# Optimization experiments

Hardware: AMD Instinct MI355X
Metric: run time of the kernel (lower is better)

The kernel has to match this reference:

```python
import jax, jax.numpy as jnp
import numpy as np

T, B, I, H = 256, 32, 128, 256
CLIP = 2.0

def setup_inputs() -> dict:
    key = jax.random.key(0)
    ks = jax.random.split(key, 10)
    si, sh = 1.0 / np.sqrt(I), 1.0 / np.sqrt(H)
    return {
        "x":     jax.random.normal(ks[0], (T, B, I), jnp.float32),
        "Wx":    jax.random.normal(ks[1], (4 * H, I), jnp.float32) * si,
        "bx":    jax.random.normal(ks[2], (4 * H,), jnp.float32) * si,
        "Wh":    jax.random.normal(ks[3], (4 * H, H), jnp.float32) * sh,
        "bh":    jax.random.normal(ks[4], (4 * H,), jnp.float32) * sh,
        "w_mod": jax.random.normal(ks[5], (1, H), jnp.float32) * sh,
        "b_mod": jax.random.normal(ks[6], (1,), jnp.float32) * sh,
        "w_fan": jax.random.normal(ks[7], (H, 1), jnp.float32),
        "b_fan": jax.random.normal(ks[8], (H,), jnp.float32),
        "alpha": 1e-4 * jax.random.uniform(ks[9], (H, H), jnp.float32),
    }

def reference(x, Wx, bx, Wh, bh, w_mod, b_mod, w_fan, b_fan, alpha):
    Bn = x.shape[1]
    # precompute input projection for all timesteps: [T, B, 4H]
    xf = jnp.einsum('tbi,gi->tbg', x, Wx) + bx

    def step(state, xf_t):
        h, c, hebb = state  # h,c: [B,H]; hebb: [B,H,H]
        fioj = xf_t + h @ Wh.T + bh                     # [B,4H]
        f = jax.nn.sigmoid(fioj[:, :H])
        i = jax.nn.sigmoid(fioj[:, H:2 * H])
        o = jax.nn.sigmoid(fioj[:, 2 * H:3 * H])
        # h_pred @ (alpha * hebb) : batched vec-mat product
        plast = jnp.einsum('bh,hk,bhk->bk', h, alpha, hebb)
        j = jnp.tanh(fioj[:, 3 * H:] + plast)
        c_new = f * c + i * j
        h_new = o * jnp.tanh(c_new)
        eta = jnp.tanh(c_new @ w_mod.T + b_mod)          # [B,1]
        myeta = eta * w_fan[:, 0] + b_fan                # [B,H] (Linear(1,H) fanout)
        # delta_hebb = outer(h_pred, j); eta modulates along the j axis
        hebb_new = jnp.clip(hebb + myeta[:, None, :] * (h[:, :, None] * j[:, None, :]),
                            -CLIP, CLIP)
        return (h_new, c_new, hebb_new), h_new

    init = (jnp.zeros((Bn, H), jnp.float32),
            jnp.zeros((Bn, H), jnp.float32),
            jnp.zeros((Bn, H, H), jnp.float32))
    (h, c, hebb), hs = jax.lax.scan(step, init, xf)
    return hs, h, c, hebb
```

## Files before the change

### kernel.cpp

```cpp
#include <hip/hip_runtime.h>


#define TT 256
#define BB 32
#define II 128
#define HH 256
#define G4 1024

typedef _Float16 h2_t __attribute__((ext_vector_type(2)));
typedef unsigned long long u64;

__device__ __forceinline__ float sigm(float x) {
    return 1.0f / (1.0f + __expf(-x));
}
__device__ __forceinline__ float tanhfast(float x) {
    return 1.0f - 2.0f / (__expf(2.0f * x) + 1.0f);
}
__device__ __forceinline__ unsigned pkh(float lo, float hi) {
    h2_t v;
    v.x = (_Float16)lo;
    v.y = (_Float16)hi;
    return __builtin_bit_cast(unsigned, v);
}

#if __has_builtin(__builtin_amdgcn_fdot2)
__device__ __forceinline__ float dot2(unsigned a, unsigned b, float c) {
    return __builtin_amdgcn_fdot2(__builtin_bit_cast(h2_t, a),
                                  __builtin_bit_cast(h2_t, b), c, false);
}
#else
__device__ __forceinline__ float dot2(unsigned a, unsigned b, float c) {
    h2_t av = __builtin_bit_cast(h2_t, a), bv = __builtin_bit_cast(h2_t, b);
    return c + (float)av.x * (float)bv.x + (float)av.y * (float)bv.y;
}
#endif

__device__ __forceinline__ h2_t pkfma(h2_t a, h2_t b, h2_t c) {
#if __has_builtin(__builtin_elementwise_fma)
    return __builtin_elementwise_fma(a, b, c);
#else
    return a * b + c;
#endif
}
__device__ __forceinline__ h2_t clip2h(h2_t x) {
    const h2_t lo = {(_Float16)-2.0f, (_Float16)-2.0f};
    const h2_t hi = {(_Float16)2.0f, (_Float16)2.0f};
#if __has_builtin(__builtin_elementwise_max) && __has_builtin(__builtin_elementwise_min)
    return __builtin_elementwise_min(__builtin_elementwise_max(x, lo), hi);
#else
    h2_t r = x;
    r.x = r.x < lo.x ? lo.x : (r.x > hi.x ? hi.x : r.x);
    r.y = r.y < lo.y ? lo.y : (r.y > hi.y ? hi.y : r.y);
    return r;
#endif
}

__global__ __launch_bounds__(256) void prep_wd3(const float* __restrict__ Wh,
                                                uint4* __restrict__ Wd3) {
    int idx = blockIdx.x * 256 + threadIdx.x;
    int ro = idx >> 12, rem = idx & 4095;
    int g = rem >> 2, ri = rem & 3;
    int r8 = 4 * ro + ri;
    const float4* s = (const float4*)(Wh + (size_t)g * HH + (r8 << 3));
    float4 a = s[0], b2 = s[1];
    uint4 o;
    o.x = pkh(a.x, a.y);
    o.y = pkh(a.z, a.w);
    o.z = pkh(b2.x, b2.y);
    o.w = pkh(b2.z, b2.w);
    Wd3[idx] = o;
}

__global__ __launch_bounds__(256) void prep_alq(const float* __restrict__ alpha,
                                                uint4* __restrict__ alQ) {
    int idx = blockIdx.x * 256 + threadIdx.x;
    int p4 = idx >> 8, k = idx & 255;
    unsigned r[4];
#pragma unroll
    for (int j = 0; j < 4; ++j) {
        int p = 4 * p4 + j;
        float a0 = alpha[(size_t)(2 * p) * HH + k];
        float a1 = alpha[(size_t)(2 * p + 1) * HH + k];
        r[j] = pkh(a0, a1);
    }
    uint4 o; o.x = r[0]; o.y = r[1]; o.z = r[2]; o.w = r[3];
    alQ[idx] = o;
}

__global__ __launch_bounds__(256) void xf_gemm(const float* __restrict__ x,
                                               const float* __restrict__ Wx,
                                               const float* __restrict__ bx,
                                               const float* __restrict__ bh,
                                               float* __restrict__ xf) {
    __shared__ float As[64][37];
    __shared__ float Bs[64][37];
    const int tid = threadIdx.x;
    const int tx = tid & 15, ty = tid >> 4;
    const int m0 = blockIdx.y << 6;
    const int n0 = blockIdx.x << 6;
    float c[4][4] = {};

    for (int k0 = 0; k0 < II; k0 += 32) {
#pragma unroll
        for (int hh = 0; hh < 2; ++hh) {
            int row = (tid >> 3) + (hh << 5);
            int col = (tid & 7) << 2;
            float4 va = *(const float4*)(x + (size_t)(m0 + row) * II + k0 + col);
            As[row][col] = va.x; As[row][col + 1] = va.y;
            As[row][col + 2] = va.z; As[row][col + 3] = va.w;
            float4 vb = *(const float4*)(Wx + (size_t)(n0 + row) * II + k0 + col);
            Bs[row][col] = vb.x; Bs[row][col + 1] = vb.y;
            Bs[row][col + 2] = vb.z; Bs[row][col + 3] = vb.w;
        }
        __syncthreads();
#pragma unroll
        for (int kk = 0; kk < 32; ++kk) {
            float a[4], bb[4];
#pragma unroll
            for (int u = 0; u < 4; ++u) a[u] = As[(ty << 2) + u][kk];
#pragma unroll
            for (int v = 0; v < 4; ++v) bb[v] = Bs[(tx << 2) + v][kk];
#pragma unroll
            for (int u = 0; u < 4; ++u)
#pragma unroll
                for (int v = 0; v < 4; ++v)
                    c[u][v] = fmaf(a[u], bb[v], c[u][v]);
        }
        __syncthreads();
    }
    const int n = n0 + (tx << 2);
    float4 bxv = *(const float4*)(bx + n);
    float4 bhv = *(const float4*)(bh + n);
    float4 badd = {bxv.x + bhv.x, bxv.y + bhv.y, bxv.z + bhv.z, bxv.w + bhv.w};
#pragma unroll
    for (int u = 0; u < 4; ++u) {
        int m = m0 + (ty << 2) + u;
        float4 o = {c[u][0] + badd.x, c[u][1] + badd.y,
                    c[u][2] + badd.z, c[u][3] + badd.w};
        *(float4*)(xf + (size_t)m * G4 + n) = o;
    }
}

#define HBQ_FOREACH(X) X(0) X(1) X(2) X(3) X(4) X(5) X(6) X(7)

#define HBQ_DECL(i) h2_t hp##i = {(_Float16)0.0f, (_Float16)0.0f};
#define HBQ_OUT(i) \
    hbout[(size_t)(r0g + 2 * i) * HH + k]     = (float)hp##i.x; \
    hbout[(size_t)(r0g + 2 * i + 1) * HH + k] = (float)hp##i.y;

#define HBQ_STEP(i, au, hou, hnu) { \
    h2_t al2 = __builtin_bit_cast(h2_t, au); \
    h2_t ho2 = __builtin_bit_cast(h2_t, hou); \
    h2_t hn2 = __builtin_bit_cast(h2_t, hnu); \
    hp##i = clip2h(pkfma(mj2, ho2, hp##i)); \
    h2_t hna = hn2 * al2; \
    pp = dot2(__builtin_bit_cast(unsigned, hna), \
              __builtin_bit_cast(unsigned, hp##i), pp); }

#define HBQ_CHUNK(q, AV, i0, i1, i2, i3) { \
    uint4 ho = hfO4[hb4 + (q)]; \
    uint4 hn = hfN4[hb4 + (q)]; \
    HBQ_STEP(i0, AV.x, ho.x, hn.x) \
    HBQ_STEP(i1, AV.y, ho.y, hn.y) \
    HBQ_STEP(i2, AV.z, ho.z, hn.z) \
    HBQ_STEP(i3, AV.w, ho.w, hn.w) }

#define HBV_STEP(i, hou) { \
    h2_t ho2 = __builtin_bit_cast(h2_t, hou); \
    hp##i = clip2h(pkfma(mj2, ho2, hp##i)); }
#define HBV_CHUNK(q, i0, i1, i2, i3) { \
    uint4 ho = hfO4[hb4 + (q)]; \
    HBV_STEP(i0, ho.x) HBV_STEP(i1, ho.y) \
    HBV_STEP(i2, ho.z) HBV_STEP(i3, ho.w) }

#define DOTW(W, HV) { \
    ac0 = dot2(W.x, HV.x, ac0); ac1 = dot2(W.y, HV.y, ac1); \
    ac2 = dot2(W.z, HV.z, ac2); ac3 = dot2(W.w, HV.w, ac3); }

__global__ __launch_bounds__(1024, 1) void scan_kernel(
    const float* __restrict__ xf,
    const uint4* __restrict__ Wd3,
    const uint4* __restrict__ alQ,
    const float* __restrict__ w_mod,
    const float* __restrict__ b_mod,
    const float* __restrict__ w_fan,
    const float* __restrict__ b_fan,
    u64* __restrict__ exData,
    float* __restrict__ out) {
    const int bid = blockIdx.x;
    const int r   = bid >> 5;
    const int b   = bid & 31;
    const int tid = threadIdx.x;
    const int k   = tid & (HH - 1);
    const int rg  = tid >> 8;
    const int r0g = r * 64 + rg * 16;
    const int hb4 = r0g >> 3;

    __shared__ alignas(16) unsigned short hf_s[2][HH];
    __shared__ float fioj_s[G4];
    __shared__ float pp_s[4][HH];
    __shared__ float red_s[4];

    HBQ_FOREACH(HBQ_DECL)

    if (tid < HH) {
        hf_s[0][tid] = 0;
        hf_s[1][tid] = 0;
    }
    if (tid < 4) red_s[tid] = 0.0f;
    __syncthreads();

    const float bmod = b_mod[0];
    const float wf = w_fan[k], bf = b_fan[k], wm = w_mod[k];
    float creg = 0.0f, jreg = 0.0f, hnreg = 0.0f;

    const uint4* wb = Wd3 + ((size_t)(2 * r) << 12) + (tid << 2);
    uint4 w0 = wb[0], w1 = wb[1], w2 = wb[2], w3 = wb[3];
    uint4 w4 = wb[4096], w5 = wb[4097], w6 = wb[4098], w7 = wb[4099];
    uint4 aqA = alQ[(size_t)(8 * r + 2 * rg) * 256 + k];
    uint4 aqB = alQ[(size_t)(8 * r + 2 * rg + 1) * 256 + k];

    const float* xfp = xf + (size_t)b * G4 + tid;

    u64* myEx = exData + (size_t)((b * 4 + r) * 2) * 1024;
    const u64* pEx1 = exData + (size_t)((b * 4 + ((r + 1) & 3)) * 2) * 1024;
    const u64* pEx2 = exData + (size_t)((b * 4 + ((r + 2) & 3)) * 2) * 1024;
    const u64* pEx3 = exData + (size_t)((b * 4 + ((r + 3) & 3)) * 2) * 1024;

    for (int t = 0; t < TT; ++t) {
        float xfv = 0.0f;
        if (rg == r) xfv = xfp[(size_t)t * BB * G4];

        float eta = tanhfast(((red_s[0] + red_s[1]) + (red_s[2] + red_s[3])) + bmod);
        float mj = fmaf(eta, wf, bf) * jreg;
        h2_t mj2;
        mj2.x = (_Float16)mj;
        mj2.y = mj2.x;
        const uint4* hfO4 = (const uint4*)hf_s[t & 1];
        const uint4* hfN4 = (const uint4*)hf_s[(t & 1) ^ 1];
        float pp = 0.0f;
        HBQ_CHUNK(0, aqA, 0, 1, 2, 3)
        HBQ_CHUNK(1, aqB, 4, 5, 6, 7)
        pp_s[rg][k] = pp;

        float ac0 = 0.f, ac1 = 0.f, ac2 = 0.f, ac3 = 0.f;
        {
            const int hx = r << 3;
            uint4 h0 = hfN4[hx], h1 = hfN4[hx + 1];
            uint4 h2 = hfN4[hx + 2], h3 = hfN4[hx + 3];
            DOTW(w0, h0) DOTW(w1, h1) DOTW(w2, h2) DOTW(w3, h3)
            uint4 h4 = hfN4[hx + 4], h5 = hfN4[hx + 5];
            uint4 h6 = hfN4[hx + 6], h7 = hfN4[hx + 7];
            DOTW(w4, h4) DOTW(w5, h5) DOTW(w6, h6) DOTW(w7, h7)
        }
        float part = ((ac0 + ac1) + (ac2 + ac3)) + xfv;
        __syncthreads();

        if (tid >= 768) {
            int k2 = tid - 768;
            part += (pp_s[0][k2] + pp_s[1][k2]) + (pp_s[2][k2] + pp_s[3][k2]);
        }

        const unsigned tag = (unsigned)(t + 1);
        const int off = (t & 1) * 1024 + tid;
        {
            u64 pkv = ((u64)tag << 32) |
                      (u64)__builtin_bit_cast(unsigned, part);
            __hip_atomic_store(&myEx[off], pkv, __ATOMIC_RELAXED,
                               __HIP_MEMORY_SCOPE_AGENT);
        }

        {
            float s1 = 0.f, s2 = 0.f, s3 = 0.f;
            bool d1 = false, d2 = false, d3 = false;
            do {
                if (!d1) {
                    u64 v = __hip_atomic_load(&pEx1[off], __ATOMIC_RELAXED,
                                              __HIP_MEMORY_SCOPE_AGENT);
                    if ((unsigned)(v >> 32) == tag) {
                        s1 = __builtin_bit_cast(float, (unsigned)v);
                        d1 = true;
                    }
                }
                if (!d2) {
                    u64 v = __hip_atomic_load(&pEx2[off], __ATOMIC_RELAXED,
                                              __HIP_MEMORY_SCOPE_AGENT);
                    if ((unsigned)(v >> 32) == tag) {
                        s2 = __builtin_bit_cast(float, (unsigned)v);
                        d2 = true;
                    }
                }
                if (!d3) {
                    u64 v = __hip_atomic_load(&pEx3[off], __ATOMIC_RELAXED,
                                              __HIP_MEMORY_SCOPE_AGENT);
                    if ((unsigned)(v >> 32) == tag) {
                        s3 = __builtin_bit_cast(float, (unsigned)v);
                        d3 = true;
                    }
                }
            } while (!(d1 && d2 && d3));
            fioj_s[tid] = part + ((s1 + s2) + s3);
        }
        __syncthreads();

        float fg = sigm(fioj_s[k]);
        float ig = sigm(fioj_s[HH + k]);
        float og = sigm(fioj_s[2 * HH + k]);
        float jp = fioj_s[3 * HH + k];
        jreg = tanhfast(jp);
        creg = fmaf(fg, creg, ig * jreg);
        hnreg = og * tanhfast(creg);
        if (rg == 0) {
            _Float16 hh = (_Float16)hnreg;
            hf_s[t & 1][k] = __builtin_bit_cast(unsigned short, hh);
            if (r == 0) out[((size_t)t * BB + b) * HH + k] = hnreg;
            float e = creg * wm;
#pragma unroll
            for (int m = 32; m >= 1; m >>= 1) e += __shfl_xor(e, m, 64);
            if ((k & 63) == 0) red_s[k >> 6] = e;
        }
        __syncthreads();
    }

    {
        float eta = tanhfast(((red_s[0] + red_s[1]) + (red_s[2] + red_s[3])) + bmod);
        float mj = fmaf(eta, wf, bf) * jreg;
        h2_t mj2;
        mj2.x = (_Float16)mj;
        mj2.y = mj2.x;
        const uint4* hfO4 = (const uint4*)hf_s[0];
        HBV_CHUNK(0, 0, 1, 2, 3)
        HBV_CHUNK(1, 4, 5, 6, 7)
    }

    const size_t HS = (size_t)TT * BB * HH;
    if (r == 0 && rg == 0) {
        out[HS + (size_t)b * HH + k]           = hnreg;
        out[HS + BB * HH + (size_t)b * HH + k] = creg;
    }
    float* hbout = out + HS + 2 * BB * HH + (size_t)b * HH * HH;
    HBQ_FOREACH(HBQ_OUT)
}

extern "C" void kernel_launch(void* const* d_in, const int* in_sizes, int n_in,
                              void* d_out, int out_size, void* d_ws,
                              size_t ws_size, hipStream_t stream) {
    const float* x     = (const float*)d_in[0];
    const float* Wx    = (const float*)d_in[1];
    const float* bx    = (const float*)d_in[2];
    const float* Wh    = (const float*)d_in[3];
    const float* bh    = (const float*)d_in[4];
    const float* w_mod = (const float*)d_in[5];
    const float* b_mod = (const float*)d_in[6];
    const float* w_fan = (const float*)d_in[7];
    const float* b_fan = (const float*)d_in[8];
    const float* alpha = (const float*)d_in[9];
    float* out = (float*)d_out;

    float* xf  = (float*)d_ws;
    uint4* Wd3 = (uint4*)((char*)d_ws + 33554432);
    uint4* alQ = (uint4*)((char*)d_ws + 34078720);
    u64*   exD = (u64*)((char*)d_ws + 34209792);

    hipLaunchKernelGGL(prep_wd3, dim3(128), dim3(256), 0, stream, Wh, Wd3);
    hipLaunchKernelGGL(prep_alq, dim3(32), dim3(256), 0, stream, alpha, alQ);
    hipLaunchKernelGGL(xf_gemm, dim3(16, 128), dim3(256), 0, stream,
                       x, Wx, bx, bh, xf);
    hipLaunchKernelGGL(scan_kernel, dim3(128), dim3(1024), 0, stream,
                       xf, Wd3, alQ, w_mod, b_mod, w_fan, b_fan,
                       exD, out);
}
```

Before: 838.5 us.

## Split each batch's recurrence across two blocks instead of four

Each batch element's scan now runs on 2 workgroups (64 total) instead of 4. Each block keeps a 128-column slice of Wh in registers (16 uint4 per thread) and stages its alpha slice in LDS. The cross-block exchange now talks to one partner, with pp partials published separately so they can be summed remotely. The next step's xf value is prefetched one step ahead. This cuts inter-block synchronisation and the number of polled locations per step, at the cost of doubled per-block dot-product and hebbian work, higher register and LDS pressure, and fewer CUs in use.

```diff
diff --git a/kernel.cpp b/kernel.cpp
--- a/kernel.cpp
+++ b/kernel.cpp
@@ -55,36 +55,29 @@
 #endif
 }
 
-__global__ __launch_bounds__(256) void prep_wd3(const float* __restrict__ Wh,
-                                                uint4* __restrict__ Wd3) {
+__global__ __launch_bounds__(256) void prep_wd2(const float* __restrict__ Wh,
+                                                uint4* __restrict__ Wd2) {
     int idx = blockIdx.x * 256 + threadIdx.x;
-    int ro = idx >> 12, rem = idx & 4095;
-    int g = rem >> 2, ri = rem & 3;
-    int r8 = 4 * ro + ri;
-    const float4* s = (const float4*)(Wh + (size_t)g * HH + (r8 << 3));
+    int Q = idx >> 10, g = idx & 1023;
+    const float4* s = (const float4*)(Wh + (size_t)g * HH + (Q << 3));
     float4 a = s[0], b2 = s[1];
     uint4 o;
     o.x = pkh(a.x, a.y);
     o.y = pkh(a.z, a.w);
     o.z = pkh(b2.x, b2.y);
     o.w = pkh(b2.z, b2.w);
-    Wd3[idx] = o;
-}
-
-__global__ __launch_bounds__(256) void prep_alq(const float* __restrict__ alpha,
-                                                uint4* __restrict__ alQ) {
+    Wd2[idx] = o;
+}
+
+__global__ __launch_bounds__(256) void prep_alp(const float* __restrict__ alpha,
+                                                unsigned* __restrict__ alP) {
     int idx = blockIdx.x * 256 + threadIdx.x;
-    int p4 = idx >> 8, k = idx & 255;
-    unsigned r[4];
-#pragma unroll
-    for (int j = 0; j < 4; ++j) {
-        int p = 4 * p4 + j;
-        float a0 = alpha[(size_t)(2 * p) * HH + k];
-        float a1 = alpha[(size_t)(2 * p + 1) * HH + k];
-        r[j] = pkh(a0, a1);
-    }
-    uint4 o; o.x = r[0]; o.y = r[1]; o.z = r[2]; o.w = r[3];
-    alQ[idx] = o;
+    int r = idx >> 14, rem = idx & 16383;
+    int j = rem & 1, kk = (rem >> 1) & 255, pg = rem >> 9;
+    int row0 = r * 128 + 4 * pg + 2 * j;
+    float a0 = alpha[(size_t)row0 * HH + kk];
+    float a1 = alpha[(size_t)(row0 + 1) * HH + kk];
+    alP[idx] = pkh(a0, a1);
 }
 
 __global__ __launch_bounds__(256) void xf_gemm(const float* __restrict__ x,
@@ -141,7 +134,8 @@
     }
 }
 
-#define HBQ_FOREACH(X) X(0) X(1) X(2) X(3) X(4) X(5) X(6) X(7)
+#define HBQ_FOREACH(X) X(0) X(1) X(2) X(3) X(4) X(5) X(6) X(7) \
+                       X(8) X(9) X(10) X(11) X(12) X(13) X(14) X(15)
 
 #define HBQ_DECL(i) h2_t hp##i = {(_Float16)0.0f, (_Float16)0.0f};
 #define HBQ_OUT(i) \
@@ -157,13 +151,15 @@
     pp = dot2(__builtin_bit_cast(unsigned, hna), \
               __builtin_bit_cast(unsigned, hp##i), pp); }
 
-#define HBQ_CHUNK(q, AV, i0, i1, i2, i3) { \
+#define HBQ_CHUNK(q, i0, i1, i2, i3) { \
     uint4 ho = hfO4[hb4 + (q)]; \
     uint4 hn = hfN4[hb4 + (q)]; \
-    HBQ_STEP(i0, AV.x, ho.x, hn.x) \
-    HBQ_STEP(i1, AV.y, ho.y, hn.y) \
-    HBQ_STEP(i2, AV.z, ho.z, hn.z) \
-    HBQ_STEP(i3, AV.w, ho.w, hn.w) }
+    uint2 A0 = *(const uint2*)&als[((((rg << 3) + 2 * (q)) << 8) + k) << 1]; \
+    uint2 A1 = *(const uint2*)&als[((((rg << 3) + 2 * (q) + 1) << 8) + k) << 1]; \
+    HBQ_STEP(i0, A0.x, ho.x, hn.x) \
+    HBQ_STEP(i1, A0.y, ho.y, hn.y) \
+    HBQ_STEP(i2, A1.x, ho.z, hn.z) \
+    HBQ_STEP(i3, A1.y, ho.w, hn.w) }
 
 #define HBV_STEP(i, hou) { \
     h2_t ho2 = __builtin_bit_cast(h2_t, hou); \
@@ -179,8 +175,8 @@
 
 __global__ __launch_bounds__(1024, 1) void scan_kernel(
     const float* __restrict__ xf,
-    const uint4* __restrict__ Wd3,
-    const uint4* __restrict__ alQ,
+    const uint4* __restrict__ Wd2,
+    const unsigned* __restrict__ alP,
     const float* __restrict__ w_mod,
     const float* __restrict__ b_mod,
     const float* __restrict__ w_fan,
@@ -193,16 +189,25 @@
     const int tid = threadIdx.x;
     const int k   = tid & (HH - 1);
     const int rg  = tid >> 8;
-    const int r0g = r * 64 + rg * 16;
-    const int hb4 = r0g >> 3;
+    const int r0g = (r << 7) + (rg << 5);
+    const int hb4 = (r << 4) + (rg << 2);
 
     __shared__ alignas(16) unsigned short hf_s[2][HH];
-    __shared__ float fioj_s[G4];
+    __shared__ alignas(16) float fioj_s[G4];
     __shared__ float pp_s[4][HH];
     __shared__ float red_s[4];
+    __shared__ alignas(16) unsigned als[16384];
 
     HBQ_FOREACH(HBQ_DECL)
 
+    {
+        const uint4* s4 = (const uint4*)(alP + ((size_t)r << 14));
+        uint4* d4 = (uint4*)als;
+        d4[tid]        = s4[tid];
+        d4[tid + 1024] = s4[tid + 1024];
+        d4[tid + 2048] = s4[tid + 2048];
+        d4[tid + 3072] = s4[tid + 3072];
+    }
     if (tid < HH) {
         hf_s[0][tid] = 0;
         hf_s[1][tid] = 0;
@@ -214,22 +219,25 @@
     const float wf = w_fan[k], bf = b_fan[k], wm = w_mod[k];
     float creg = 0.0f, jreg = 0.0f, hnreg = 0.0f;
 
-    const uint4* wb = Wd3 + ((size_t)(2 * r) << 12) + (tid << 2);
-    uint4 w0 = wb[0], w1 = wb[1], w2 = wb[2], w3 = wb[3];
-    uint4 w4 = wb[4096], w5 = wb[4097], w6 = wb[4098], w7 = wb[4099];
-    uint4 aqA = alQ[(size_t)(8 * r + 2 * rg) * 256 + k];
-    uint4 aqB = alQ[(size_t)(8 * r + 2 * rg + 1) * 256 + k];
-
+    const uint4* wb = Wd2 + ((size_t)r << 14) + tid;
+    uint4 w0 = wb[0],      w1 = wb[1024],  w2 = wb[2048],  w3 = wb[3072];
+    uint4 w4 = wb[4096],   w5 = wb[5120],  w6 = wb[6144],  w7 = wb[7168];
+    uint4 w8 = wb[8192],   w9 = wb[9216],  w10 = wb[10240], w11 = wb[11264];
+    uint4 w12 = wb[12288], w13 = wb[13312], w14 = wb[14336], w15 = wb[15360];
+
+    const bool hasxf = ((tid >> 9) == r);
     const float* xfp = xf + (size_t)b * G4 + tid;
-
-    u64* myEx = exData + (size_t)((b * 4 + r) * 2) * 1024;
-    const u64* pEx1 = exData + (size_t)((b * 4 + ((r + 1) & 3)) * 2) * 1024;
-    const u64* pEx2 = exData + (size_t)((b * 4 + ((r + 2) & 3)) * 2) * 1024;
-    const u64* pEx3 = exData + (size_t)((b * 4 + ((r + 3) & 3)) * 2) * 1024;
+    float xcur = hasxf ? xfp[0] : 0.0f;
+
+    u64* myEx = exData + ((size_t)(b * 2 + r) << 12);
+    const u64* pEx = exData + ((size_t)(b * 2 + (r ^ 1)) << 12);
 
     for (int t = 0; t < TT; ++t) {
-        float xfv = 0.0f;
-        if (rg == r) xfv = xfp[(size_t)t * BB * G4];
+        float xnext = 0.0f;
+        if (hasxf && t + 1 < TT) xnext = xfp[(size_t)(t + 1) * BB * G4];
+
+        const unsigned tag = (unsigned)(t + 1);
+        const int off = (t & 1) * 2048;
 
         float eta = tanhfast(((red_s[0] + red_s[1]) + (red_s[2] + red_s[3])) + bmod);
         float mj = fmaf(eta, wf, bf) * jreg;
@@ -239,43 +247,70 @@
         const uint4* hfO4 = (const uint4*)hf_s[t & 1];
         const uint4* hfN4 = (const uint4*)hf_s[(t & 1) ^ 1];
         float pp = 0.0f;
-        HBQ_CHUNK(0, aqA, 0, 1, 2, 3)
-        HBQ_CHUNK(1, aqB, 4, 5, 6, 7)
+        HBQ_CHUNK(0, 0, 1, 2, 3)
+        HBQ_CHUNK(1, 4, 5, 6, 7)
+        HBQ_CHUNK(2, 8, 9, 10, 11)
+        HBQ_CHUNK(3, 12, 13, 14, 15)
         pp_s[rg][k] = pp;
+        __hip_atomic_store(&myEx[off + 1024 + tid],
+                           ((u64)tag << 32) |
+                               (u64)__builtin_bit_cast(unsigned, pp),
+                           __ATOMIC_RELAXED, __HIP_MEMORY_SCOPE_AGENT);
 
         float ac0 = 0.f, ac1 = 0.f, ac2 = 0.f, ac3 = 0.f;
         {
-            const int hx = r << 3;
-            uint4 h0 = hfN4[hx], h1 = hfN4[hx + 1];
-            uint4 h2 = hfN4[hx + 2], h3 = hfN4[hx + 3];
-            DOTW(w0, h0) DOTW(w1, h1) DOTW(w2, h2) DOTW(w3, h3)
-            uint4 h4 = hfN4[hx + 4], h5 = hfN4[hx + 5];
-            uint4 h6 = hfN4[hx + 6], h7 = hfN4[hx + 7];
-            DOTW(w4, h4) DOTW(w5, h5) DOTW(w6, h6) DOTW(w7, h7)
+            const uint4* hv = hfN4 + (r << 4);
+            uint4 hA = hv[0], hB = hv[1];
+            DOTW(w0, hA) DOTW(w1, hB)
+            hA = hv[2]; hB = hv[3];
+            DOTW(w2, hA) DOTW(w3, hB)
+            hA = hv[4]; hB = hv[5];
+            DOTW(w4, hA) DOTW(w5, hB)
+            hA = hv[6]; hB = hv[7];
+            DOTW(w6, hA) DOTW(w7, hB)
+            hA = hv[8]; hB = hv[9];
+            DOTW(w8, hA) DOTW(w9, hB)
+            hA = hv[10]; hB = hv[11];
+            DOTW(w10, hA) DOTW(w11, hB)
+            hA = hv[12]; hB = hv[13];
+            DOTW(w12, hA) DOTW(w13, hB)
+            hA = hv[14]; hB = hv[15];
+            DOTW(w14, hA) DOTW(w15, hB)
         }
-        float part = ((ac0 + ac1) + (ac2 + ac3)) + xfv;
+        float part = ((ac0 + ac1) + (ac2 + ac3)) + xcur;
+        xcur = xnext;
+
+        __hip_atomic_store(&myEx[off + tid],
+                           ((u64)tag << 32) |
+                               (u64)__builtin_bit_cast(unsigned, part),
+                           __ATOMIC_RELAXED, __HIP_MEMORY_SCOPE_AGENT);
         __syncthreads();
 
-        if (tid >= 768) {
-            int k2 = tid - 768;
-            part += (pp_s[0][k2] + pp_s[1][k2]) + (pp_s[2][k2] + pp_s[3][k2]);
-        }
-
-        const unsigned tag = (unsigned)(t + 1);
-        const int off = (t & 1) * 1024 + tid;
-        {
-            u64 pkv = ((u64)tag << 32) |
-                      (u64)__builtin_bit_cast(unsigned, part);
-            __hip_atomic_store(&myEx[off], pkv, __ATOMIC_RELAXED,
-                               __HIP_MEMORY_SCOPE_AGENT);
-        }
-
-        {
-            float s1 = 0.f, s2 = 0.f, s3 = 0.f;
-            bool d1 = false, d2 = false, d3 = false;
+        float fv;
+        if (tid < 768) {
+            u64 v;
+            for (;;) {
+                v = __hip_atomic_load(&pEx[off + tid], __ATOMIC_RELAXED,
+                                      __HIP_MEMORY_SCOPE_AGENT);
+                if ((unsigned)(v >> 32) == tag) break;
+            }
+            fv = part + __builtin_bit_cast(float, (unsigned)v);
+        } else {
+            float own = (pp_s[0][k] + pp_s[1][k]) + (pp_s[2][k] + pp_s[3][k]);
+            float s0 = 0.f, s1 = 0.f, s2 = 0.f, s3 = 0.f, s4 = 0.f;
+            bool d0 = false, d1 = false, d2 = false, d3 = false, d4 = false;
             do {
+                if (!d0) {
+                    u64 v = __hip_atomic_load(&pEx[off + tid], __ATOMIC_RELAXED,
+                                              __HIP_MEMORY_SCOPE_AGENT);
+                    if ((unsigned)(v >> 32) == tag) {
+                        s0 = __builtin_bit_cast(float, (unsigned)v);
+                        d0 = true;
+                    }
+                }
                 if (!d1) {
-                    u64 v = __hip_atomic_load(&pEx1[off], __ATOMIC_RELAXED,
+                    u64 v = __hip_atomic_load(&pEx[off + 1024 + k],
+                                              __ATOMIC_RELAXED,
                                               __HIP_MEMORY_SCOPE_AGENT);
                     if ((unsigned)(v >> 32) == tag) {
                         s1 = __builtin_bit_cast(float, (unsigned)v);
@@ -283,7 +318,8 @@
                     }
                 }
                 if (!d2) {
-                    u64 v = __hip_atomic_load(&pEx2[off], __ATOMIC_RELAXED,
+                    u64 v = __hip_atomic_load(&pEx[off + 1280 + k],
+                                              __ATOMIC_RELAXED,
                                               __HIP_MEMORY_SCOPE_AGENT);
                     if ((unsigned)(v >> 32) == tag) {
                         s2 = __builtin_bit_cast(float, (unsigned)v);
@@ -291,16 +327,27 @@
                     }
                 }
                 if (!d3) {
-                    u64 v = __hip_atomic_load(&pEx3[off], __ATOMIC_RELAXED,
+                    u64 v = __hip_atomic_load(&pEx[off + 1536 + k],
+                                              __ATOMIC_RELAXED,
                                               __HIP_MEMORY_SCOPE_AGENT);
                     if ((unsigned)(v >> 32) == tag) {
                         s3 = __builtin_bit_cast(float, (unsigned)v);
                         d3 = true;
                     }
                 }
-            } while (!(d1 && d2 && d3));
-            fioj_s[tid] = part + ((s1 + s2) + s3);
+                if (!d4) {
+                    u64 v = __hip_atomic_load(&pEx[off + 1792 + k],
+                                              __ATOMIC_RELAXED,
+                                              __HIP_MEMORY_SCOPE_AGENT);
+                    if ((unsigned)(v >> 32) == tag) {
+                        s4 = __builtin_bit_cast(float, (unsigned)v);
+                        d4 = true;
+                    }
+                }
+            } while (!(d0 && d1 && d2 && d3 && d4));
+            fv = (part + own) + (((s0 + s1) + (s2 + s3)) + s4);
         }
+        fioj_s[tid] = fv;
         __syncthreads();
 
         float fg = sigm(fioj_s[k]);
@@ -331,6 +378,8 @@
         const uint4* hfO4 = (const uint4*)hf_s[0];
         HBV_CHUNK(0, 0, 1, 2, 3)
         HBV_CHUNK(1, 4, 5, 6, 7)
+        HBV_CHUNK(2, 8, 9, 10, 11)
+        HBV_CHUNK(3, 12, 13, 14, 15)
     }
 
     const size_t HS = (size_t)TT * BB * HH;
@@ -357,16 +406,16 @@
     const float* alpha = (const float*)d_in[9];
     float* out = (float*)d_out;
 
-    float* xf  = (float*)d_ws;
-    uint4* Wd3 = (uint4*)((char*)d_ws + 33554432);
-    uint4* alQ = (uint4*)((char*)d_ws + 34078720);
-    u64*   exD = (u64*)((char*)d_ws + 34209792);
-
-    hipLaunchKernelGGL(prep_wd3, dim3(128), dim3(256), 0, stream, Wh, Wd3);
-    hipLaunchKernelGGL(prep_alq, dim3(32), dim3(256), 0, stream, alpha, alQ);
+    float*    xf  = (float*)d_ws;
+    uint4*    Wd2 = (uint4*)((char*)d_ws + 33554432);
+    unsigned* alP = (unsigned*)((char*)d_ws + 34078720);
+    u64*      exD = (u64*)((char*)d_ws + 34209792);
+
+    hipLaunchKernelGGL(prep_wd2, dim3(128), dim3(256), 0, stream, Wh, Wd2);
+    hipLaunchKernelGGL(prep_alp, dim3(128), dim3(256), 0, stream, alpha, alP);
     hipLaunchKernelGGL(xf_gemm, dim3(16, 128), dim3(256), 0, stream,
                        x, Wx, bx, bh, xf);
-    hipLaunchKernelGGL(scan_kernel, dim3(128), dim3(1024), 0, stream,
-                       xf, Wd3, alQ, w_mod, b_mod, w_fan, b_fan,
+    hipLaunchKernelGGL(scan_kernel, dim3(64), dim3(1024), 0, stream,
+                       xf, Wd2, alP, w_mod, b_mod, w_fan, b_fan,
                        exD, out);
 }
```

Result: slower. 1.088 ms (+29.7%).

## Speed up cross-block exchange with dual-buffer publish and sc0 polling loads

Applied to the files above, without the earlier changes.

Each partial sum is now written twice, once with workgroup scope to a second buffer and once with agent scope to the original buffer. Peers poll the fast buffer with inline-asm sc0 global loads and fall back to agent-scope atomic loads every fourth iteration. The non-plastic partials are published before the block barrier, the next timestep's xf value is prefetched, and gate math is limited to the threads that use it. The goal is lower inter-block handshake latency per step, but it relies on cache-coherence behaviour that is not formally guaranteed and adds extra stores and workspace.

```diff
diff --git a/kernel.cpp b/kernel.cpp
--- a/kernel.cpp
+++ b/kernel.cpp
@@ -53,6 +53,18 @@
     r.y = r.y < lo.y ? lo.y : (r.y > hi.y ? hi.y : r.y);
     return r;
 #endif
+}
+
+__device__ __forceinline__ void ld3_fast(const u64* p1, const u64* p2,
+                                         const u64* p3,
+                                         u64& v1, u64& v2, u64& v3) {
+    asm volatile(
+        "global_load_dwordx2 %0, %3, off sc0\n\t"
+        "global_load_dwordx2 %1, %4, off sc0\n\t"
+        "global_load_dwordx2 %2, %5, off sc0\n\t"
+        "s_waitcnt vmcnt(0)"
+        : "=&v"(v1), "=&v"(v2), "=&v"(v3)
+        : "v"(p1), "v"(p2), "v"(p3));
 }
 
 __global__ __launch_bounds__(256) void prep_wd3(const float* __restrict__ Wh,
@@ -177,6 +189,13 @@
     ac0 = dot2(W.x, HV.x, ac0); ac1 = dot2(W.y, HV.y, ac1); \
     ac2 = dot2(W.z, HV.z, ac2); ac3 = dot2(W.w, HV.w, ac3); }
 
+#define PUBLISH(val) { \
+    u64 pkv = ((u64)tag << 32) | (u64)__builtin_bit_cast(unsigned, val); \
+    __hip_atomic_store(&myF[off], pkv, __ATOMIC_RELAXED, \
+                       __HIP_MEMORY_SCOPE_WORKGROUP); \
+    __hip_atomic_store(&myEx[off], pkv, __ATOMIC_RELAXED, \
+                       __HIP_MEMORY_SCOPE_AGENT); }
+
 __global__ __launch_bounds__(1024, 1) void scan_kernel(
     const float* __restrict__ xf,
     const uint4* __restrict__ Wd3,
@@ -186,6 +205,7 @@
     const float* __restrict__ w_fan,
     const float* __restrict__ b_fan,
     u64* __restrict__ exData,
+    u64* __restrict__ exFast,
     float* __restrict__ out) {
     const int bid = blockIdx.x;
     const int r   = bid >> 5;
@@ -221,15 +241,23 @@
     uint4 aqB = alQ[(size_t)(8 * r + 2 * rg + 1) * 256 + k];
 
     const float* xfp = xf + (size_t)b * G4 + tid;
+    float xcur = (rg == r) ? xfp[0] : 0.0f;
 
     u64* myEx = exData + (size_t)((b * 4 + r) * 2) * 1024;
     const u64* pEx1 = exData + (size_t)((b * 4 + ((r + 1) & 3)) * 2) * 1024;
     const u64* pEx2 = exData + (size_t)((b * 4 + ((r + 2) & 3)) * 2) * 1024;
     const u64* pEx3 = exData + (size_t)((b * 4 + ((r + 3) & 3)) * 2) * 1024;
+    u64* myF = exFast + (size_t)((b * 4 + r) * 2) * 1024;
+    const u64* pF1 = exFast + (size_t)((b * 4 + ((r + 1) & 3)) * 2) * 1024;
+    const u64* pF2 = exFast + (size_t)((b * 4 + ((r + 2) & 3)) * 2) * 1024;
+    const u64* pF3 = exFast + (size_t)((b * 4 + ((r + 3) & 3)) * 2) * 1024;
 
     for (int t = 0; t < TT; ++t) {
-        float xfv = 0.0f;
-        if (rg == r) xfv = xfp[(size_t)t * BB * G4];
+        float xnext = 0.0f;
+        if (rg == r && t + 1 < TT) xnext = xfp[(size_t)(t + 1) * BB * G4];
+
+        const unsigned tag = (unsigned)(t + 1);
+        const int off = (t & 1) * 1024 + tid;
 
         float eta = tanhfast(((red_s[0] + red_s[1]) + (red_s[2] + red_s[3])) + bmod);
         float mj = fmaf(eta, wf, bf) * jreg;
@@ -253,64 +281,62 @@
             uint4 h6 = hfN4[hx + 6], h7 = hfN4[hx + 7];
             DOTW(w4, h4) DOTW(w5, h5) DOTW(w6, h6) DOTW(w7, h7)
         }
-        float part = ((ac0 + ac1) + (ac2 + ac3)) + xfv;
+        float part = ((ac0 + ac1) + (ac2 + ac3)) + xcur;
+        xcur = xnext;
+
+        if (tid < 768) PUBLISH(part)
         __syncthreads();
 
         if (tid >= 768) {
             int k2 = tid - 768;
             part += (pp_s[0][k2] + pp_s[1][k2]) + (pp_s[2][k2] + pp_s[3][k2]);
-        }
-
-        const unsigned tag = (unsigned)(t + 1);
-        const int off = (t & 1) * 1024 + tid;
-        {
-            u64 pkv = ((u64)tag << 32) |
-                      (u64)__builtin_bit_cast(unsigned, part);
-            __hip_atomic_store(&myEx[off], pkv, __ATOMIC_RELAXED,
-                               __HIP_MEMORY_SCOPE_AGENT);
+            PUBLISH(part)
         }
 
         {
             float s1 = 0.f, s2 = 0.f, s3 = 0.f;
             bool d1 = false, d2 = false, d3 = false;
+            const u64* f1 = pF1 + off;
+            const u64* f2 = pF2 + off;
+            const u64* f3 = pF3 + off;
+            int it = 0;
             do {
-                if (!d1) {
-                    u64 v = __hip_atomic_load(&pEx1[off], __ATOMIC_RELAXED,
-                                              __HIP_MEMORY_SCOPE_AGENT);
-                    if ((unsigned)(v >> 32) == tag) {
-                        s1 = __builtin_bit_cast(float, (unsigned)v);
-                        d1 = true;
-                    }
+                u64 v1, v2, v3;
+                if ((it & 3) != 3) {
+                    ld3_fast(f1, f2, f3, v1, v2, v3);
+                } else {
+                    v1 = __hip_atomic_load(pEx1 + off, __ATOMIC_RELAXED,
+                                           __HIP_MEMORY_SCOPE_AGENT);
+                    v2 = __hip_atomic_load(pEx2 + off, __ATOMIC_RELAXED,
+                                           __HIP_MEMORY_SCOPE_AGENT);
+                    v3 = __hip_atomic_load(pEx3 + off, __ATOMIC_RELAXED,
+                                           __HIP_MEMORY_SCOPE_AGENT);
                 }
-                if (!d2) {
-                    u64 v = __hip_atomic_load(&pEx2[off], __ATOMIC_RELAXED,
-                                              __HIP_MEMORY_SCOPE_AGENT);
-                    if ((unsigned)(v >> 32) == tag) {
-                        s2 = __builtin_bit_cast(float, (unsigned)v);
-                        d2 = true;
-                    }
+                ++it;
+                if (!d1 && (unsigned)(v1 >> 32) == tag) {
+                    s1 = __builtin_bit_cast(float, (unsigned)v1);
+                    d1 = true;
                 }
-                if (!d3) {
-                    u64 v = __hip_atomic_load(&pEx3[off], __ATOMIC_RELAXED,
-                                              __HIP_MEMORY_SCOPE_AGENT);
-                    if ((unsigned)(v >> 32) == tag) {
-                        s3 = __builtin_bit_cast(float, (unsigned)v);
-                        d3 = true;
-                    }
+                if (!d2 && (unsigned)(v2 >> 32) == tag) {
+                    s2 = __builtin_bit_cast(float, (unsigned)v2);
+                    d2 = true;
+                }
+                if (!d3 && (unsigned)(v3 >> 32) == tag) {
+                    s3 = __builtin_bit_cast(float, (unsigned)v3);
+                    d3 = true;
                 }
             } while (!(d1 && d2 && d3));
             fioj_s[tid] = part + ((s1 + s2) + s3);
         }
         __syncthreads();
 
-        float fg = sigm(fioj_s[k]);
-        float ig = sigm(fioj_s[HH + k]);
-        float og = sigm(fioj_s[2 * HH + k]);
-        float jp = fioj_s[3 * HH + k];
-        jreg = tanhfast(jp);
-        creg = fmaf(fg, creg, ig * jreg);
-        hnreg = og * tanhfast(creg);
+        jreg = tanhfast(fioj_s[3 * HH + k]);
         if (rg == 0) {
+            float fg = sigm(fioj_s[k]);
+            float ig = sigm(fioj_s[HH + k]);
+            float og = sigm(fioj_s[2 * HH + k]);
+            creg = fmaf(fg, creg, ig * jreg);
+            hnreg = og * tanhfast(creg);
             _Float16 hh = (_Float16)hnreg;
             hf_s[t & 1][k] = __builtin_bit_cast(unsigned short, hh);
             if (r == 0) out[((size_t)t * BB + b) * HH + k] = hnreg;
@@ -361,6 +387,7 @@
     uint4* Wd3 = (uint4*)((char*)d_ws + 33554432);
     uint4* alQ = (uint4*)((char*)d_ws + 34078720);
     u64*   exD = (u64*)((char*)d_ws + 34209792);
+    u64*   exF = (u64*)((char*)d_ws + 36306944);
 
     hipLaunchKernelGGL(prep_wd3, dim3(128), dim3(256), 0, stream, Wh, Wd3);
     hipLaunchKernelGGL(prep_alq, dim3(32), dim3(256), 0, stream, alpha, alQ);
@@ -368,5 +395,5 @@
                        x, Wx, bx, bh, xf);
     hipLaunchKernelGGL(scan_kernel, dim3(128), dim3(1024), 0, stream,
                        xf, Wd3, alQ, w_mod, b_mod, w_fan, b_fan,
-                       exD, out);
-}
+                       exD, exF, out);
+}
```

Measured after the change: 757.5 us. -9.7%, faster.

## Split scan by hidden-unit slices and exchange packed h instead of gate partials

Applied to the files above, without the earlier changes.

Each of the 4 blocks per batch row now owns 64 hidden units across all four gates, using the full K dimension of Wh. The old scheme split the K dimension and exchanged 1024 gate partial sums per step through global memory. Now only the 64 fp16 h values (packed in pairs) and one eta partial per block are published, and a few dedicated threads spin on them using a sc0 fast-path load with a periodic agent-scope fallback. xf is prefetched four steps at a time into LDS, and Wh is repacked to match the new ownership. This cuts inter-block traffic per step sharply, but it serializes the gate math onto 64 threads and depends on inline-asm cache semantics for correctness of the spin.

```diff
diff --git a/kernel.cpp b/kernel.cpp
--- a/kernel.cpp
+++ b/kernel.cpp
@@ -55,20 +55,36 @@
 #endif
 }
 
-__global__ __launch_bounds__(256) void prep_wd3(const float* __restrict__ Wh,
-                                                uint4* __restrict__ Wd3) {
+__device__ __forceinline__ u64 spin_slot(const u64* fp, const u64* dp,
+                                         unsigned tag) {
+    u64 v;
+    int it = 0;
+    for (;;) {
+        if ((it & 3) == 3) {
+            v = __hip_atomic_load(dp, __ATOMIC_RELAXED,
+                                  __HIP_MEMORY_SCOPE_AGENT);
+        } else {
+            asm volatile("global_load_dwordx2 %0, %1, off sc0\n\t"
+                         "s_waitcnt vmcnt(0)"
+                         : "=v"(v) : "v"(fp));
+        }
+        ++it;
+        if ((unsigned)(v >> 32) == tag) return v;
+    }
+}
+
+__global__ __launch_bounds__(256) void prep_wdx(const float* __restrict__ Wh,
+                                                uint4* __restrict__ Wd) {
     int idx = blockIdx.x * 256 + threadIdx.x;
-    int ro = idx >> 12, rem = idx & 4095;
-    int g = rem >> 2, ri = rem & 3;
-    int r8 = 4 * ro + ri;
-    const float4* s = (const float4*)(Wh + (size_t)g * HH + (r8 << 3));
+    int c = idx >> 10, g = idx & 1023;
+    const float4* s = (const float4*)(Wh + (size_t)g * HH + (c << 3));
     float4 a = s[0], b2 = s[1];
     uint4 o;
     o.x = pkh(a.x, a.y);
     o.y = pkh(a.z, a.w);
     o.z = pkh(b2.x, b2.y);
     o.w = pkh(b2.z, b2.w);
-    Wd3[idx] = o;
+    Wd[idx] = o;
 }
 
 __global__ __launch_bounds__(256) void prep_alq(const float* __restrict__ alpha,
@@ -145,8 +161,8 @@
 
 #define HBQ_DECL(i) h2_t hp##i = {(_Float16)0.0f, (_Float16)0.0f};
 #define HBQ_OUT(i) \
-    hbout[(size_t)(r0g + 2 * i) * HH + k]     = (float)hp##i.x; \
-    hbout[(size_t)(r0g + 2 * i + 1) * HH + k] = (float)hp##i.y;
+    hbout[(size_t)((rr << 4) + 2 * i) * HH + kcol]     = (float)hp##i.x; \
+    hbout[(size_t)((rr << 4) + 2 * i + 1) * HH + kcol] = (float)hp##i.y;
 
 #define HBQ_STEP(i, au, hou, hnu) { \
     h2_t al2 = __builtin_bit_cast(h2_t, au); \
@@ -177,28 +193,41 @@
     ac0 = dot2(W.x, HV.x, ac0); ac1 = dot2(W.y, HV.y, ac1); \
     ac2 = dot2(W.z, HV.z, ac2); ac3 = dot2(W.w, HV.w, ac3); }
 
+#define PUB(slotoff, val32) { \
+    u64 pkv = ((u64)tag << 32) | (u64)(val32); \
+    __hip_atomic_store(&myF[slotoff], pkv, __ATOMIC_RELAXED, \
+                       __HIP_MEMORY_SCOPE_WORKGROUP); \
+    __hip_atomic_store(&myEx[slotoff], pkv, __ATOMIC_RELAXED, \
+                       __HIP_MEMORY_SCOPE_AGENT); }
+
 __global__ __launch_bounds__(1024, 1) void scan_kernel(
     const float* __restrict__ xf,
-    const uint4* __restrict__ Wd3,
+    const uint4* __restrict__ Wd,
     const uint4* __restrict__ alQ,
     const float* __restrict__ w_mod,
     const float* __restrict__ b_mod,
     const float* __restrict__ w_fan,
     const float* __restrict__ b_fan,
     u64* __restrict__ exData,
+    u64* __restrict__ exFast,
     float* __restrict__ out) {
     const int bid = blockIdx.x;
     const int r   = bid >> 5;
     const int b   = bid & 31;
     const int tid = threadIdx.x;
-    const int k   = tid & (HH - 1);
-    const int rg  = tid >> 8;
-    const int r0g = r * 64 + rg * 16;
-    const int hb4 = r0g >> 3;
+    const int kk  = tid >> 8;
+    const int m   = tid & 255;
+    const int g   = ((m >> 6) << 8) + (r << 6) + (m & 63);
+    const int rr  = tid >> 6;
+    const int ch6 = tid & 63;
+    const int kcol = (r << 6) + ch6;
+    const int hb4 = rr << 1;
 
     __shared__ alignas(16) unsigned short hf_s[2][HH];
-    __shared__ float fioj_s[G4];
-    __shared__ float pp_s[4][HH];
+    __shared__ float part_s[G4];
+    __shared__ float pp_s[G4];
+    __shared__ alignas(16) float xfs[4][256];
+    __shared__ float js[64];
     __shared__ float red_s[4];
 
     HBQ_FOREACH(HBQ_DECL)
@@ -208,44 +237,58 @@
         hf_s[1][tid] = 0;
     }
     if (tid < 4) red_s[tid] = 0.0f;
+    if (tid < 64) js[tid] = 0.0f;
     __syncthreads();
 
     const float bmod = b_mod[0];
-    const float wf = w_fan[k], bf = b_fan[k], wm = w_mod[k];
-    float creg = 0.0f, jreg = 0.0f, hnreg = 0.0f;
-
-    const uint4* wb = Wd3 + ((size_t)(2 * r) << 12) + (tid << 2);
-    uint4 w0 = wb[0], w1 = wb[1], w2 = wb[2], w3 = wb[3];
-    uint4 w4 = wb[4096], w5 = wb[4097], w6 = wb[4098], w7 = wb[4099];
-    uint4 aqA = alQ[(size_t)(8 * r + 2 * rg) * 256 + k];
-    uint4 aqB = alQ[(size_t)(8 * r + 2 * rg + 1) * 256 + k];
-
-    const float* xfp = xf + (size_t)b * G4 + tid;
-
-    u64* myEx = exData + (size_t)((b * 4 + r) * 2) * 1024;
-    const u64* pEx1 = exData + (size_t)((b * 4 + ((r + 1) & 3)) * 2) * 1024;
-    const u64* pEx2 = exData + (size_t)((b * 4 + ((r + 2) & 3)) * 2) * 1024;
-    const u64* pEx3 = exData + (size_t)((b * 4 + ((r + 3) & 3)) * 2) * 1024;
+    const float wfq = w_fan[kcol], bfq = b_fan[kcol];
+    const float wmq = w_mod[kcol];
+    float creg = 0.0f, hreg = 0.0f;
+
+    const uint4* wb = Wd + ((size_t)(kk << 3) << 10) + g;
+    uint4 w0 = wb[0],    w1 = wb[1024], w2 = wb[2048], w3 = wb[3072];
+    uint4 w4 = wb[4096], w5 = wb[5120], w6 = wb[6144], w7 = wb[7168];
+    uint4 aqA = alQ[(size_t)(hb4) * 256 + kcol];
+    uint4 aqB = alQ[(size_t)(hb4 + 1) * 256 + kcol];
+
+    u64* myEx = exData + ((size_t)(b * 4 + r) << 7);
+    u64* myF  = exFast + ((size_t)(b * 4 + r) << 7);
+    const int rp1 = (r + 1) & 3, rp2 = (r + 2) & 3, rp3 = (r + 3) & 3;
+    const u64* pEx[3] = {exData + ((size_t)(b * 4 + rp1) << 7),
+                         exData + ((size_t)(b * 4 + rp2) << 7),
+                         exData + ((size_t)(b * 4 + rp3) << 7)};
+    const u64* pF[3]  = {exFast + ((size_t)(b * 4 + rp1) << 7),
+                         exFast + ((size_t)(b * 4 + rp2) << 7),
+                         exFast + ((size_t)(b * 4 + rp3) << 7)};
+    const int prole[3] = {rp1, rp2, rp3};
 
     for (int t = 0; t < TT; ++t) {
-        float xfv = 0.0f;
-        if (rg == r) xfv = xfp[(size_t)t * BB * G4];
+        const unsigned tag = (unsigned)(t + 1);
+        const int sb = (t & 1) << 6;
+
+        if ((t & 3) == 0) {
+            const int d = tid >> 8;
+            const int mm = tid & 255;
+            const int gg = ((mm >> 6) << 8) + (r << 6) + (mm & 63);
+            xfs[d][mm] = xf[(size_t)(t + d) * BB * G4 + (size_t)b * G4 + gg];
+        }
+
+        const uint4* hfO4 = (const uint4*)hf_s[t & 1];
+        const uint4* hfN4 = (const uint4*)hf_s[(t & 1) ^ 1];
 
         float eta = tanhfast(((red_s[0] + red_s[1]) + (red_s[2] + red_s[3])) + bmod);
-        float mj = fmaf(eta, wf, bf) * jreg;
+        float mj = fmaf(eta, wfq, bfq) * js[ch6];
         h2_t mj2;
         mj2.x = (_Float16)mj;
         mj2.y = mj2.x;
-        const uint4* hfO4 = (const uint4*)hf_s[t & 1];
-        const uint4* hfN4 = (const uint4*)hf_s[(t & 1) ^ 1];
         float pp = 0.0f;
         HBQ_CHUNK(0, aqA, 0, 1, 2, 3)
         HBQ_CHUNK(1, aqB, 4, 5, 6, 7)
-        pp_s[rg][k] = pp;
+        pp_s[tid] = pp;
 
         float ac0 = 0.f, ac1 = 0.f, ac2 = 0.f, ac3 = 0.f;
         {
-            const int hx = r << 3;
+            const int hx = kk << 3;
             uint4 h0 = hfN4[hx], h1 = hfN4[hx + 1];
             uint4 h2 = hfN4[hx + 2], h3 = hfN4[hx + 3];
             DOTW(w0, h0) DOTW(w1, h1) DOTW(w2, h2) DOTW(w3, h3)
@@ -253,78 +296,76 @@
             uint4 h6 = hfN4[hx + 6], h7 = hfN4[hx + 7];
             DOTW(w4, h4) DOTW(w5, h5) DOTW(w6, h6) DOTW(w7, h7)
         }
-        float part = ((ac0 + ac1) + (ac2 + ac3)) + xfv;
+        part_s[tid] = ((ac0 + ac1) + (ac2 + ac3));
         __syncthreads();
 
-        if (tid >= 768) {
-            int k2 = tid - 768;
-            part += (pp_s[0][k2] + pp_s[1][k2]) + (pp_s[2][k2] + pp_s[3][k2]);
-        }
-
-        const unsigned tag = (unsigned)(t + 1);
-        const int off = (t & 1) * 1024 + tid;
-        {
-            u64 pkv = ((u64)tag << 32) |
-                      (u64)__builtin_bit_cast(unsigned, part);
-            __hip_atomic_store(&myEx[off], pkv, __ATOMIC_RELAXED,
-                               __HIP_MEMORY_SCOPE_AGENT);
-        }
-
-        {
-            float s1 = 0.f, s2 = 0.f, s3 = 0.f;
-            bool d1 = false, d2 = false, d3 = false;
-            do {
-                if (!d1) {
-                    u64 v = __hip_atomic_load(&pEx1[off], __ATOMIC_RELAXED,
-                                              __HIP_MEMORY_SCOPE_AGENT);
-                    if ((unsigned)(v >> 32) == tag) {
-                        s1 = __builtin_bit_cast(float, (unsigned)v);
-                        d1 = true;
-                    }
-                }
-                if (!d2) {
-                    u64 v = __hip_atomic_load(&pEx2[off], __ATOMIC_RELAXED,
-                                              __HIP_MEMORY_SCOPE_AGENT);
-                    if ((unsigned)(v >> 32) == tag) {
-                        s2 = __builtin_bit_cast(float, (unsigned)v);
-                        d2 = true;
-                    }
-                }
-                if (!d3) {
-                    u64 v = __hip_atomic_load(&pEx3[off], __ATOMIC_RELAXED,
-                                              __HIP_MEMORY_SCOPE_AGENT);
-                    if ((unsigned)(v >> 32) == tag) {
-                        s3 = __builtin_bit_cast(float, (unsigned)v);
-                        d3 = true;
-                    }
-                }
-            } while (!(d1 && d2 && d3));
-            fioj_s[tid] = part + ((s1 + s2) + s3);
-        }
-        __syncthreads();
-
-        float fg = sigm(fioj_s[k]);
-        float ig = sigm(fioj_s[HH + k]);
-        float og = sigm(fioj_s[2 * HH + k]);
-        float jp = fioj_s[3 * HH + k];
-        jreg = tanhfast(jp);
-        creg = fmaf(fg, creg, ig * jreg);
-        hnreg = og * tanhfast(creg);
-        if (rg == 0) {
-            _Float16 hh = (_Float16)hnreg;
-            hf_s[t & 1][k] = __builtin_bit_cast(unsigned short, hh);
-            if (r == 0) out[((size_t)t * BB + b) * HH + k] = hnreg;
-            float e = creg * wm;
-#pragma unroll
-            for (int m = 32; m >= 1; m >>= 1) e += __shfl_xor(e, m, 64);
-            if ((k & 63) == 0) red_s[k >> 6] = e;
+        if (tid < 64) {
+            const int c6 = tid;
+            float s0 = ((part_s[c6] + part_s[256 + c6]) +
+                        (part_s[512 + c6] + part_s[768 + c6])) +
+                       xfs[t & 3][c6];
+            float s1 = ((part_s[64 + c6] + part_s[320 + c6]) +
+                        (part_s[576 + c6] + part_s[832 + c6])) +
+                       xfs[t & 3][64 + c6];
+            float s2 = ((part_s[128 + c6] + part_s[384 + c6]) +
+                        (part_s[640 + c6] + part_s[896 + c6])) +
+                       xfs[t & 3][128 + c6];
+            float s3 = ((part_s[192 + c6] + part_s[448 + c6]) +
+                        (part_s[704 + c6] + part_s[960 + c6])) +
+                       xfs[t & 3][192 + c6];
+            float p01 = (pp_s[c6] + pp_s[64 + c6]) +
+                        (pp_s[128 + c6] + pp_s[192 + c6]);
+            float p23 = (pp_s[256 + c6] + pp_s[320 + c6]) +
+                        (pp_s[384 + c6] + pp_s[448 + c6]);
+            float p45 = (pp_s[512 + c6] + pp_s[576 + c6]) +
+                        (pp_s[640 + c6] + pp_s[704 + c6]);
+            float p67 = (pp_s[768 + c6] + pp_s[832 + c6]) +
+                        (pp_s[896 + c6] + pp_s[960 + c6]);
+            s3 += (p01 + p23) + (p45 + p67);
+
+            float fg = sigm(s0);
+            float ig = sigm(s1);
+            float og = sigm(s2);
+            float jv = tanhfast(s3);
+            creg = fmaf(fg, creg, ig * jv);
+            hreg = og * tanhfast(creg);
+            js[c6] = jv;
+            _Float16 hh = (_Float16)hreg;
+            unsigned hu = (unsigned)__builtin_bit_cast(unsigned short, hh);
+            hf_s[t & 1][(r << 6) + c6] = (unsigned short)hu;
+            out[((size_t)t * BB + b) * HH + (r << 6) + c6] = hreg;
+
+            float e = creg * wmq;
+#pragma unroll
+            for (int mm = 32; mm >= 1; mm >>= 1) e += __shfl_xor(e, mm, 64);
+
+            unsigned other = (unsigned)__shfl_xor((int)hu, 1, 64);
+            if ((c6 & 1) == 0) {
+                unsigned pay = hu | (other << 16);
+                PUB(sb + (c6 >> 1), pay)
+            }
+            if (c6 == 0) {
+                red_s[r] = e;
+                PUB(sb + 32, __builtin_bit_cast(unsigned, e))
+            }
+        }
+
+        if (tid >= 64 && tid < 160) {
+            const int p = (tid - 64) >> 5;
+            const int s = (tid - 64) & 31;
+            u64 v = spin_slot(pF[p] + sb + s, pEx[p] + sb + s, tag);
+            ((unsigned*)hf_s[t & 1])[(prole[p] << 5) + s] = (unsigned)v;
+        } else if (tid >= 160 && tid < 163) {
+            const int p = tid - 160;
+            u64 v = spin_slot(pF[p] + sb + 32, pEx[p] + sb + 32, tag);
+            red_s[prole[p]] = __builtin_bit_cast(float, (unsigned)v);
         }
         __syncthreads();
     }
 
     {
         float eta = tanhfast(((red_s[0] + red_s[1]) + (red_s[2] + red_s[3])) + bmod);
-        float mj = fmaf(eta, wf, bf) * jreg;
+        float mj = fmaf(eta, wfq, bfq) * js[ch6];
         h2_t mj2;
         mj2.x = (_Float16)mj;
         mj2.y = mj2.x;
@@ -334,9 +375,9 @@
     }
 
     const size_t HS = (size_t)TT * BB * HH;
-    if (r == 0 && rg == 0) {
-        out[HS + (size_t)b * HH + k]           = hnreg;
-        out[HS + BB * HH + (size_t)b * HH + k] = creg;
+    if (tid < 64) {
+        out[HS + (size_t)b * HH + kcol]           = hreg;
+        out[HS + BB * HH + (size_t)b * HH + kcol] = creg;
     }
     float* hbout = out + HS + 2 * BB * HH + (size_t)b * HH * HH;
     HBQ_FOREACH(HBQ_OUT)
@@ -358,15 +399,16 @@
     float* out = (float*)d_out;
 
     float* xf  = (float*)d_ws;
-    uint4* Wd3 = (uint4*)((char*)d_ws + 33554432);
+    uint4* Wd  = (uint4*)((char*)d_ws + 33554432);
     uint4* alQ = (uint4*)((char*)d_ws + 34078720);
     u64*   exD = (u64*)((char*)d_ws + 34209792);
-
-    hipLaunchKernelGGL(prep_wd3, dim3(128), dim3(256), 0, stream, Wh, Wd3);
+    u64*   exF = (u64*)((char*)d_ws + 34340864);
+
+    hipLaunchKernelGGL(prep_wdx, dim3(128), dim3(256), 0, stream, Wh, Wd);
     hipLaunchKernelGGL(prep_alq, dim3(32), dim3(256), 0, stream, alpha, alQ);
     hipLaunchKernelGGL(xf_gemm, dim3(16, 128), dim3(256), 0, stream,
                        x, Wx, bx, bh, xf);
     hipLaunchKernelGGL(scan_kernel, dim3(128), dim3(1024), 0, stream,
-                       xf, Wd3, alQ, w_mod, b_mod, w_fan, b_fan,
-                       exD, out);
-}
+                       xf, Wd, alQ, w_mod, b_mod, w_fan, b_fan,
+                       exD, exF, out);
+}
```

Result: faster. 796.5 us (-5.0%).
